# Performance work log

Measured on AMD Instinct MI355X. Metric: run time of the kernel, lower is better.

The kernel has to match this reference:

```python
import jax, jax.numpy as jnp
import numpy as np

N = 50000      # nodes
E = 800000     # edges (avg degree 16)
H = 128        # hidden
ED = 64        # edge_dim
L = 3          # num_layers
LN_EPS = 1e-5


def setup_inputs() -> dict:
    key = jax.random.key(0)
    ks = jax.random.split(key, 12)
    s = jax.random.normal(ks[0], (N, H), dtype=jnp.float32)
    edge_index = jax.random.randint(ks[1], (2, E), 0, N, dtype=jnp.int32)
    edge_attr = jax.random.normal(ks[2], (E, ED), dtype=jnp.float32)
    sc = 0.02
    We = sc * jax.random.normal(ks[3], (L, ED, H), dtype=jnp.float32)
    be = sc * jax.random.normal(ks[4], (L, H), dtype=jnp.float32)
    W1 = sc * jax.random.normal(ks[5], (L, H, H), dtype=jnp.float32)
    b1 = sc * jax.random.normal(ks[6], (L, H), dtype=jnp.float32)
    W2 = sc * jax.random.normal(ks[7], (L, H, H), dtype=jnp.float32)
    b2 = sc * jax.random.normal(ks[8], (L, H), dtype=jnp.float32)
    gamma = jnp.ones((L, H), dtype=jnp.float32)
    beta = jnp.zeros((L, H), dtype=jnp.float32)
    return {"s": s, "edge_index": edge_index, "edge_attr": edge_attr,
            "We": We, "be": be, "W1": W1, "b1": b1, "W2": W2, "b2": b2,
            "gamma": gamma, "beta": beta}


def reference(s, edge_index, edge_attr, We, be, W1, b1, W2, b2, gamma, beta):
    src = edge_index[0]  # j (source of message)
    dst = edge_index[1]  # i (target / aggregation index)
    for l in range(L):
        # GINEConv: message = relu(x_j + Lin(edge_attr)); sum-aggregate; eps=0
        e = edge_attr @ We[l] + be[l]                       # [E, H]
        msg = jax.nn.relu(s[src] + e)                       # [E, H] gather + fuse
        agg = jax.ops.segment_sum(msg, dst, num_segments=N)  # [N, H] scatter-add
        h = s + agg                                         # (1+eps)*x + aggr, eps=0
        h = jax.nn.silu(h @ W1[l] + b1[l]) @ W2[l] + b2[l]   # GINE MLP
        s = s + h                                           # residual
        mu = jnp.mean(s, axis=-1, keepdims=True)
        var = jnp.var(s, axis=-1, keepdims=True)
        s = (s - mu) * jax.lax.rsqrt(var + LN_EPS) * gamma[l] + beta[l]
        s = jax.nn.silu(s)
        # dropout p=0.0 / eval mode -> identity
    return s
```

## Files before the change

### kernel.cpp

```cpp
#include <hip/hip_runtime.h>
#include <hip/hip_bf16.h>

#define HH 128
#define EDD 64
#define NLAYER 3
#define LN_EPS 1e-5f
#define LROW 136

typedef __attribute__((ext_vector_type(8))) __bf16 bf16x8;
typedef __attribute__((ext_vector_type(4))) float f32x4;

static __device__ __forceinline__ float bf2f(unsigned short u) {
    return __uint_as_float(((unsigned)u) << 16);
}
static __device__ __forceinline__ unsigned short f2bf(float f) {
    return __builtin_bit_cast(unsigned short, (__bf16)f);
}
static __device__ __forceinline__ float silu(float x) {
    return x / (1.f + __expf(-x));
}

__global__ __launch_bounds__(256) void hist_kernel(
    const int* __restrict__ dst, int* __restrict__ cnt, int E)
{
    for (int e = blockIdx.x * blockDim.x + threadIdx.x; e < E;
         e += gridDim.x * blockDim.x)
        atomicAdd(&cnt[dst[e]], 1);
}

__global__ __launch_bounds__(1024) void scan_kernel(
    int* __restrict__ cnt_cursor, int* __restrict__ off, int N)
{
    __shared__ int ls[1024];
    const int t = threadIdx.x;
    const int C = (N + 1023) >> 10;
    const int lo = t * C;
    const int hi = min(lo + C, N);
    int sum = 0;
    for (int i = lo; i < hi; ++i) sum += cnt_cursor[i];
    ls[t] = sum;
    __syncthreads();
    for (int d = 1; d < 1024; d <<= 1) {
        int v = (t >= d) ? ls[t - d] : 0;
        __syncthreads();
        ls[t] += v;
        __syncthreads();
    }
    int excl = (t == 0) ? 0 : ls[t - 1];
    for (int i = lo; i < hi; ++i) {
        const int c = cnt_cursor[i];
        off[i] = excl;
        cnt_cursor[i] = excl;
        excl += c;
    }
    if (t == 1023) off[N] = ls[1023];
}

__global__ __launch_bounds__(256) void scatter2_kernel(
    const int* __restrict__ src, const int* __restrict__ dst,
    int* __restrict__ cursor, int* __restrict__ src_s,
    int* __restrict__ eid_s, int E)
{
    if (blockIdx.x == 0 && threadIdx.x < 16) {
        src_s[E + threadIdx.x] = 0;
        eid_s[E + threadIdx.x] = 0;
    }
    for (int e = blockIdx.x * blockDim.x + threadIdx.x; e < E;
         e += gridDim.x * blockDim.x) {
        const int pos = atomicAdd(&cursor[dst[e]], 1);
        src_s[pos] = src[e];
        eid_s[pos] = e;
    }
}

__global__ __launch_bounds__(256) void conv_ea(
    const float* __restrict__ ea, unsigned short* __restrict__ ea_b,
    long long total4)
{
    for (long long i = blockIdx.x * 256LL + threadIdx.x; i < total4;
         i += gridDim.x * 256LL) {
        const float4 v = reinterpret_cast<const float4*>(ea)[i];
        ushort4 o;
        o.x = f2bf(v.x); o.y = f2bf(v.y); o.z = f2bf(v.z); o.w = f2bf(v.w);
        reinterpret_cast<ushort4*>(ea_b)[i] = o;
    }
}

__global__ __launch_bounds__(256) void conv_s(
    const float* __restrict__ s0, unsigned int* __restrict__ sbp,
    long long total4)
{
    for (long long i = blockIdx.x * 256LL + threadIdx.x; i < total4;
         i += gridDim.x * 256LL) {
        const float4 v = reinterpret_cast<const float4*>(s0)[i];
        const unsigned a = (unsigned)f2bf(v.x) | ((unsigned)f2bf(v.y) << 16);
        const unsigned b = (unsigned)f2bf(v.z) | ((unsigned)f2bf(v.w) << 16);
        reinterpret_cast<uint2*>(sbp)[i] = make_uint2(a, b);
    }
}

__global__ void prep_we(const float* __restrict__ We, bf16x8* __restrict__ WeB)
{
    const int t = blockIdx.x * blockDim.x + threadIdx.x;
    if (t >= NLAYER * 16 * 64) return;
    const int lane  = t & 63;
    const int frag  = (t >> 6) & 15;
    const int layer = t >> 10;
    const int kt = frag >> 3, ct = frag & 7;
    const int col = ct * 16 + (lane & 15);
    const int k0  = kt * 32 + (lane >> 4) * 8;
    bf16x8 v;
    #pragma unroll
    for (int j = 0; j < 8; ++j)
        v[j] = (__bf16)We[(long long)layer * EDD * HH + (k0 + j) * HH + col];
    WeB[t] = v;
}

__global__ void prep_w128(const float* __restrict__ W, bf16x8* __restrict__ WB)
{
    const int t = blockIdx.x * blockDim.x + threadIdx.x;
    if (t >= NLAYER * 32 * 64) return;
    const int lane  = t & 63;
    const int frag  = (t >> 6) & 31;
    const int layer = t >> 11;
    const int kt = frag >> 3, ct = frag & 7;
    const int col = ct * 16 + (lane & 15);
    const int k0  = kt * 32 + (lane >> 4) * 8;
    bf16x8 v;
    #pragma unroll
    for (int j = 0; j < 8; ++j)
        v[j] = (__bf16)W[(long long)layer * HH * HH + (k0 + j) * HH + col];
    WB[t] = v;
}

__global__ __launch_bounds__(256, 3) void gine_agg_mfma(
    const float* __restrict__ s,
    const unsigned short* __restrict__ sb,
    const int* __restrict__ src_s,
    const int* __restrict__ eid_s,
    const int* __restrict__ off,
    const unsigned short* __restrict__ ea_b,
    const bf16x8* __restrict__ WeB,
    const float* __restrict__ be,
    unsigned short* __restrict__ hb16,
    int N, int E)
{
    __shared__ unsigned short lsb[2][16 * LROW];

    const int tid  = threadIdx.x;
    const int wave = tid >> 6;
    const int half = wave & 1;
    const int slot = wave >> 1;
    const int lane = tid & 63;
    const int lmod = lane & 15;
    const int ldiv = lane >> 4;

    bf16x8 wb0[4], wb1[4];
    #pragma unroll
    for (int c = 0; c < 4; ++c) {
        wb0[c] = WeB[(0 * 8 + half * 4 + c) * 64 + lane];
        wb1[c] = WeB[(1 * 8 + half * 4 + c) * 64 + lane];
    }
    float bev[4];
    #pragma unroll
    for (int c = 0; c < 4; ++c) bev[c] = be[(half * 4 + c) * 16 + lmod];

    const int st_slot = tid >> 7;
    const int st_row  = (tid >> 3) & 15;
    const int st_su   = (tid & 7) * 16;

    const int stride = gridDim.x * 2;
    int base = blockIdx.x * 2;
    if (base >= N) return;

    int n0 = base;
    int n1 = min(base + 1, N - 1);
    int q0 = off[n0], q0e = off[n0 + 1];
    int q1 = off[n1], q1e = off[n1 + 1];
    int p0  = slot ? q1 : q0;
    int p1  = slot ? q1e : q0e;
    int sp0 = st_slot ? q1 : q0;
    int iters = max(1, max((q0e - q0 + 15) >> 4, (q1e - q1 + 15) >> 4));

    {
        const int snode = src_s[min(sp0 + st_row, E + 15)];
        const unsigned short* srow0 = &sb[(long long)snode * HH + st_su];
        uint4 va = *reinterpret_cast<const uint4*>(srow0);
        uint4 vb = *reinterpret_cast<const uint4*>(srow0 + 8);
        const int rowid = eid_s[min(p0 + lmod, E + 15)];
        const unsigned short* ar = ea_b + (long long)rowid * EDD + ldiv * 8;
        bf16x8 a0 = *reinterpret_cast<const bf16x8*>(ar);
        bf16x8 a1 = *reinterpret_cast<const bf16x8*>(ar + 32);

        while (true) {
            const int nbase = base + stride;
            int nq0 = 0, nq0e = 0, nq1 = 0, nq1e = 0;
            if (nbase < N) {
                const int m0 = nbase, m1 = min(nbase + 1, N - 1);
                nq0 = off[m0]; nq0e = off[m0 + 1];
                nq1 = off[m1]; nq1e = off[m1 + 1];
            }
            const int myn = slot ? n1 : n0;

            float acc[4] = {0.f, 0.f, 0.f, 0.f};

            for (int it = 0; it < iters; ++it) {
                __syncthreads();
                unsigned short* drow = &lsb[st_slot][st_row * LROW + st_su];
                *reinterpret_cast<uint4*>(drow)     = va;
                *reinterpret_cast<uint4*>(drow + 8) = vb;

                uint4 nva = va, nvb = vb;
                bf16x8 na0 = a0, na1 = a1;
                if (it + 1 < iters) {
                    const int ns = src_s[min(sp0 + (it + 1) * 16 + st_row, E + 15)];
                    const unsigned short* nsr = &sb[(long long)ns * HH + st_su];
                    nva = *reinterpret_cast<const uint4*>(nsr);
                    nvb = *reinterpret_cast<const uint4*>(nsr + 8);
                    const int nr = eid_s[min(p0 + (it + 1) * 16 + lmod, E + 15)];
                    const unsigned short* nar = ea_b + (long long)nr * EDD + ldiv * 8;
                    na0 = *reinterpret_cast<const bf16x8*>(nar);
                    na1 = *reinterpret_cast<const bf16x8*>(nar + 32);
                } else if (nbase < N) {
                    const int nsp0 = st_slot ? nq1 : nq0;
                    const int np0  = slot ? nq1 : nq0;
                    const int ns = src_s[min(nsp0 + st_row, E + 15)];
                    const unsigned short* nsr = &sb[(long long)ns * HH + st_su];
                    nva = *reinterpret_cast<const uint4*>(nsr);
                    nvb = *reinterpret_cast<const uint4*>(nsr + 8);
                    const int nr = eid_s[min(np0 + lmod, E + 15)];
                    const unsigned short* nar = ea_b + (long long)nr * EDD + ldiv * 8;
                    na0 = *reinterpret_cast<const bf16x8*>(nar);
                    na1 = *reinterpret_cast<const bf16x8*>(nar + 32);
                }

                f32x4 cf[4];
                #pragma unroll
                for (int c = 0; c < 4; ++c) {
                    f32x4 z = {0.f, 0.f, 0.f, 0.f};
                    z = __builtin_amdgcn_mfma_f32_16x16x32_bf16(a0, wb0[c], z, 0, 0, 0);
                    z = __builtin_amdgcn_mfma_f32_16x16x32_bf16(a1, wb1[c], z, 0, 0, 0);
                    cf[c] = z;
                }

                __syncthreads();

                const int rem = p1 - (p0 + it * 16);
                #pragma unroll
                for (int r = 0; r < 4; ++r) {
                    if (ldiv * 4 + r < rem) {
                        const unsigned short* lr = &lsb[slot][(ldiv * 4 + r) * LROW];
                        #pragma unroll
                        for (int c = 0; c < 4; ++c)
                            acc[c] += fmaxf(
                                bf2f(lr[(half * 4 + c) * 16 + lmod]) + cf[c][r] + bev[c],
                                0.f);
                    }
                }

                va = nva; vb = nvb; a0 = na0; a1 = na1;
            }

            #pragma unroll
            for (int c = 0; c < 4; ++c) {
                acc[c] += __shfl_xor(acc[c], 16, 64);
                acc[c] += __shfl_xor(acc[c], 32, 64);
            }
            const float av = (ldiv == 0) ? acc[0] : (ldiv == 1) ? acc[1]
                           : (ldiv == 2) ? acc[2] : acc[3];
            const int col = (half * 4 + ldiv) * 16 + lmod;
            const long long nb = (long long)myn * HH;
            hb16[nb + col] = f2bf(s[nb + col] + av);

            if (nbase >= N) break;
            base = nbase;
            n0 = base; n1 = min(base + 1, N - 1);
            q0 = nq0; q0e = nq0e; q1 = nq1; q1e = nq1e;
            p0  = slot ? q1 : q0;
            p1  = slot ? q1e : q0e;
            sp0 = st_slot ? q1 : q0;
            iters = max(1, max((q0e - q0 + 15) >> 4, (q1e - q1 + 15) >> 4));
        }
    }
}

__global__ __launch_bounds__(256) void gine_mlp(
    const float* __restrict__ s_in,
    const unsigned short* __restrict__ h16,
    const bf16x8* __restrict__ W1B, const float* __restrict__ b1,
    const bf16x8* __restrict__ W2B, const float* __restrict__ b2,
    const float* __restrict__ gamma, const float* __restrict__ beta,
    float* __restrict__ s_out,
    unsigned short* __restrict__ sb_out,
    int N)
{
    __shared__ unsigned short t1t[16 * LROW];
    __shared__ float2 red[4][16];

    const int wave = threadIdx.x >> 6;
    const int lane = threadIdx.x & 63;
    const int lmod = lane & 15;
    const int ldiv = lane >> 4;

    bf16x8 wf1[4][2], wf2[4][2];
    #pragma unroll
    for (int kt = 0; kt < 4; ++kt) {
        wf1[kt][0] = W1B[(kt * 8 + 2 * wave    ) * 64 + lane];
        wf1[kt][1] = W1B[(kt * 8 + 2 * wave + 1) * 64 + lane];
        wf2[kt][0] = W2B[(kt * 8 + 2 * wave    ) * 64 + lane];
        wf2[kt][1] = W2B[(kt * 8 + 2 * wave + 1) * 64 + lane];
    }
    float4 b1v[2], b2v[2], gv[2], ev[2];
    #pragma unroll
    for (int ctl = 0; ctl < 2; ++ctl) {
        const int oc0 = (2 * wave + ctl) * 16 + ldiv * 4;
        b1v[ctl] = *reinterpret_cast<const float4*>(&b1[oc0]);
        b2v[ctl] = *reinterpret_cast<const float4*>(&b2[oc0]);
        gv[ctl]  = *reinterpret_cast<const float4*>(&gamma[oc0]);
        ev[ctl]  = *reinterpret_cast<const float4*>(&beta[oc0]);
    }

    const int ntiles = (N + 15) >> 4;
    for (int t = blockIdx.x; t < ntiles; t += gridDim.x) {
        const int node = t * 16 + lmod;
        const long long nb = (long long)min(node, N - 1) * HH;

        f32x4 c0 = {0.f, 0.f, 0.f, 0.f};
        f32x4 c1 = {0.f, 0.f, 0.f, 0.f};
        #pragma unroll
        for (int kt = 0; kt < 4; ++kt) {
            const bf16x8 hf = *reinterpret_cast<const bf16x8*>(
                &h16[nb + kt * 32 + ldiv * 8]);
            c0 = __builtin_amdgcn_mfma_f32_16x16x32_bf16(wf1[kt][0], hf, c0, 0, 0, 0);
            c1 = __builtin_amdgcn_mfma_f32_16x16x32_bf16(wf1[kt][1], hf, c1, 0, 0, 0);
        }
        #pragma unroll
        for (int ctl = 0; ctl < 2; ++ctl) {
            const f32x4 cc = ctl ? c1 : c0;
            const float4 bb = ctl ? b1v[1] : b1v[0];
            uint2 pk;
            pk.x = (unsigned)f2bf(silu(cc[0] + bb.x)) |
                   ((unsigned)f2bf(silu(cc[1] + bb.y)) << 16);
            pk.y = (unsigned)f2bf(silu(cc[2] + bb.z)) |
                   ((unsigned)f2bf(silu(cc[3] + bb.w)) << 16);
            const int oc0 = (2 * wave + ctl) * 16 + ldiv * 4;
            *reinterpret_cast<uint2*>(&t1t[lmod * LROW + oc0]) = pk;
        }
        __syncthreads();

        f32x4 d0 = {0.f, 0.f, 0.f, 0.f};
        f32x4 d1 = {0.f, 0.f, 0.f, 0.f};
        #pragma unroll
        for (int kt = 0; kt < 4; ++kt) {
            const bf16x8 tf = *reinterpret_cast<const bf16x8*>(
                &t1t[lmod * LROW + kt * 32 + ldiv * 8]);
            d0 = __builtin_amdgcn_mfma_f32_16x16x32_bf16(wf2[kt][0], tf, d0, 0, 0, 0);
            d1 = __builtin_amdgcn_mfma_f32_16x16x32_bf16(wf2[kt][1], tf, d1, 0, 0, 0);
        }

        float v[2][4];
        float sum = 0.f, ssq = 0.f;
        #pragma unroll
        for (int ctl = 0; ctl < 2; ++ctl) {
            const int oc0 = (2 * wave + ctl) * 16 + ldiv * 4;
            const float4 sv = *reinterpret_cast<const float4*>(&s_in[nb + oc0]);
            const f32x4 dd = ctl ? d1 : d0;
            const float4 bb = ctl ? b2v[1] : b2v[0];
            v[ctl][0] = sv.x + dd[0] + bb.x;
            v[ctl][1] = sv.y + dd[1] + bb.y;
            v[ctl][2] = sv.z + dd[2] + bb.z;
            v[ctl][3] = sv.w + dd[3] + bb.w;
            #pragma unroll
            for (int r = 0; r < 4; ++r) { sum += v[ctl][r]; ssq += v[ctl][r] * v[ctl][r]; }
        }
        sum += __shfl_xor(sum, 16, 64); sum += __shfl_xor(sum, 32, 64);
        ssq += __shfl_xor(ssq, 16, 64); ssq += __shfl_xor(ssq, 32, 64);
        if (ldiv == 0) red[wave][lmod] = make_float2(sum, ssq);
        __syncthreads();
        float ts = 0.f, tq = 0.f;
        #pragma unroll
        for (int w = 0; w < 4; ++w) {
            const float2 rr = red[w][lmod];
            ts += rr.x; tq += rr.y;
        }
        __syncthreads();

        const float mu = ts * (1.0f / HH);
        const float var = tq * (1.0f / HH) - mu * mu;
        const float rs = rsqrtf(var + LN_EPS);

        if (node < N) {
            #pragma unroll
            for (int ctl = 0; ctl < 2; ++ctl) {
                const int oc0 = (2 * wave + ctl) * 16 + ldiv * 4;
                float o[4];
                o[0] = silu((v[ctl][0] - mu) * rs * gv[ctl].x + ev[ctl].x);
                o[1] = silu((v[ctl][1] - mu) * rs * gv[ctl].y + ev[ctl].y);
                o[2] = silu((v[ctl][2] - mu) * rs * gv[ctl].z + ev[ctl].z);
                o[3] = silu((v[ctl][3] - mu) * rs * gv[ctl].w + ev[ctl].w);
                *reinterpret_cast<float4*>(&s_out[nb + oc0]) =
                    make_float4(o[0], o[1], o[2], o[3]);
                uint2 pk;
                pk.x = (unsigned)f2bf(o[0]) | ((unsigned)f2bf(o[1]) << 16);
                pk.y = (unsigned)f2bf(o[2]) | ((unsigned)f2bf(o[3]) << 16);
                *reinterpret_cast<uint2*>(&sb_out[nb + oc0]) = pk;
            }
        }
    }
}

extern "C" void kernel_launch(void* const* d_in, const int* in_sizes, int n_in,
                              void* d_out, int out_size, void* d_ws, size_t ws_size,
                              hipStream_t stream) {
    const float* s0  = (const float*)d_in[0];
    const int*   ei  = (const int*)  d_in[1];
    const float* ea  = (const float*)d_in[2];
    const float* We  = (const float*)d_in[3];
    const float* be  = (const float*)d_in[4];
    const float* W1  = (const float*)d_in[5];
    const float* b1  = (const float*)d_in[6];
    const float* W2  = (const float*)d_in[7];
    const float* b2  = (const float*)d_in[8];
    const float* gm  = (const float*)d_in[9];
    const float* bt  = (const float*)d_in[10];

    const int NH = in_sizes[0];
    const int N  = NH / HH;
    const int E  = in_sizes[1] / 2;
    const int* src = ei;
    const int* dst = ei + E;

    float*          sbuf  = (float*)d_ws;
    unsigned short* sb    = (unsigned short*)(sbuf + NH);
    unsigned short* hb16  = sb + NH;
    unsigned short* ea_b  = hb16 + NH;
    bf16x8*         WeB   = (bf16x8*)(ea_b + (size_t)E * EDD);
    bf16x8*         W1B   = WeB + NLAYER * 16 * 64;
    bf16x8*         W2B   = W1B + NLAYER * 32 * 64;
    int*            src_s = (int*)(W2B + NLAYER * 32 * 64);
    int*            eid_s = src_s + (E + 16);
    int*            off   = eid_s + (E + 16);
    int*            cursor= off + (N + 1);

    hipMemsetAsync(cursor, 0, sizeof(int) * N, stream);
    hist_kernel<<<1024, 256, 0, stream>>>(dst, cursor, E);
    scan_kernel<<<1, 1024, 0, stream>>>(cursor, off, N);
    scatter2_kernel<<<1024, 256, 0, stream>>>(src, dst, cursor, src_s, eid_s, E);
    conv_ea<<<2048, 256, 0, stream>>>(ea, ea_b, (long long)E * EDD / 4);
    conv_s<<<1024, 256, 0, stream>>>(s0, (unsigned int*)sb, (long long)NH / 4);
    prep_we<<<12, 256, 0, stream>>>(We, WeB);
    prep_w128<<<24, 256, 0, stream>>>(W1, W1B);
    prep_w128<<<24, 256, 0, stream>>>(W2, W2B);

    for (int l = 0; l < NLAYER; ++l) {
        const float* scur = (l == 0) ? s0 : sbuf;
        gine_agg_mfma<<<4096, 256, 0, stream>>>(scur, sb, src_s, eid_s, off, ea_b,
                                                WeB + (size_t)l * 16 * 64,
                                                be + l * HH, hb16, N, E);
        float* sout = (l == NLAYER - 1) ? (float*)d_out : sbuf;
        gine_mlp<<<2048, 256, 0, stream>>>(scur, hb16,
                                           W1B + (size_t)l * 32 * 64, b1 + l * HH,
                                           W2B + (size_t)l * 32 * 64, b2 + l * HH,
                                           gm + l * HH, bt + l * HH,
                                           sout, sb, N);
    }
}
```

Baseline: 615.5 us.

## Store bf16 edge attributes in destination-sorted order, drop edge-id indirection

The edge-attribute conversion now writes each bf16 row to its CSR (dst-sorted) position, using a per-edge position array recorded during the scatter pass. The aggregation kernel then reads edge attributes contiguously by sorted position instead of gathering through an edge-id array. This removes one indirect index load and turns random 128-byte row gathers into sequential reads in each of the three layers. The cost is a scattered write in the one-time conversion kernel, and 16 padding rows that must be zeroed with an extra memset.

```diff
diff --git a/kernel.cpp b/kernel.cpp
--- a/kernel.cpp
+++ b/kernel.cpp
@@ -56,33 +56,31 @@
     if (t == 1023) off[N] = ls[1023];
 }
 
-__global__ __launch_bounds__(256) void scatter2_kernel(
+__global__ __launch_bounds__(256) void scatter3_kernel(
     const int* __restrict__ src, const int* __restrict__ dst,
     int* __restrict__ cursor, int* __restrict__ src_s,
-    int* __restrict__ eid_s, int E)
-{
-    if (blockIdx.x == 0 && threadIdx.x < 16) {
+    int* __restrict__ pos_e, int E)
+{
+    if (blockIdx.x == 0 && threadIdx.x < 16)
         src_s[E + threadIdx.x] = 0;
-        eid_s[E + threadIdx.x] = 0;
-    }
     for (int e = blockIdx.x * blockDim.x + threadIdx.x; e < E;
          e += gridDim.x * blockDim.x) {
         const int pos = atomicAdd(&cursor[dst[e]], 1);
         src_s[pos] = src[e];
-        eid_s[pos] = e;
-    }
-}
-
-__global__ __launch_bounds__(256) void conv_ea(
-    const float* __restrict__ ea, unsigned short* __restrict__ ea_b,
-    long long total4)
-{
-    for (long long i = blockIdx.x * 256LL + threadIdx.x; i < total4;
-         i += gridDim.x * 256LL) {
-        const float4 v = reinterpret_cast<const float4*>(ea)[i];
-        ushort4 o;
-        o.x = f2bf(v.x); o.y = f2bf(v.y); o.z = f2bf(v.z); o.w = f2bf(v.w);
-        reinterpret_cast<ushort4*>(ea_b)[i] = o;
+        pos_e[e] = pos;
+    }
+}
+
+__global__ __launch_bounds__(256) void conv_ea_sorted(
+    const float* __restrict__ ea, const int* __restrict__ pos_e,
+    unsigned short* __restrict__ ea_s, int E)
+{
+    const int wave = threadIdx.x >> 6;
+    const int lane = threadIdx.x & 63;
+    for (int e = blockIdx.x * 4 + wave; e < E; e += gridDim.x * 4) {
+        const float v = ea[(long long)e * EDD + lane];
+        const int pos = pos_e[e];
+        ea_s[(long long)pos * EDD + lane] = f2bf(v);
     }
 }
 
@@ -137,9 +135,8 @@
     const float* __restrict__ s,
     const unsigned short* __restrict__ sb,
     const int* __restrict__ src_s,
-    const int* __restrict__ eid_s,
     const int* __restrict__ off,
-    const unsigned short* __restrict__ ea_b,
+    const unsigned short* __restrict__ ea_s,
     const bf16x8* __restrict__ WeB,
     const float* __restrict__ be,
     unsigned short* __restrict__ hb16,
@@ -187,8 +184,8 @@
         const unsigned short* srow0 = &sb[(long long)snode * HH + st_su];
         uint4 va = *reinterpret_cast<const uint4*>(srow0);
         uint4 vb = *reinterpret_cast<const uint4*>(srow0 + 8);
-        const int rowid = eid_s[min(p0 + lmod, E + 15)];
-        const unsigned short* ar = ea_b + (long long)rowid * EDD + ldiv * 8;
+        const unsigned short* ar =
+            ea_s + (long long)min(p0 + lmod, E + 15) * EDD + ldiv * 8;
         bf16x8 a0 = *reinterpret_cast<const bf16x8*>(ar);
         bf16x8 a1 = *reinterpret_cast<const bf16x8*>(ar + 32);
 
@@ -217,8 +214,9 @@
                     const unsigned short* nsr = &sb[(long long)ns * HH + st_su];
                     nva = *reinterpret_cast<const uint4*>(nsr);
                     nvb = *reinterpret_cast<const uint4*>(nsr + 8);
-                    const int nr = eid_s[min(p0 + (it + 1) * 16 + lmod, E + 15)];
-                    const unsigned short* nar = ea_b + (long long)nr * EDD + ldiv * 8;
+                    const unsigned short* nar =
+                        ea_s + (long long)min(p0 + (it + 1) * 16 + lmod, E + 15) * EDD
+                        + ldiv * 8;
                     na0 = *reinterpret_cast<const bf16x8*>(nar);
                     na1 = *reinterpret_cast<const bf16x8*>(nar + 32);
                 } else if (nbase < N) {
@@ -228,8 +226,8 @@
                     const unsigned short* nsr = &sb[(long long)ns * HH + st_su];
                     nva = *reinterpret_cast<const uint4*>(nsr);
                     nvb = *reinterpret_cast<const uint4*>(nsr + 8);
-                    const int nr = eid_s[min(np0 + lmod, E + 15)];
-                    const unsigned short* nar = ea_b + (long long)nr * EDD + ldiv * 8;
+                    const unsigned short* nar =
+                        ea_s + (long long)min(np0 + lmod, E + 15) * EDD + ldiv * 8;
                     na0 = *reinterpret_cast<const bf16x8*>(nar);
                     na1 = *reinterpret_cast<const bf16x8*>(nar + 32);
                 }
@@ -433,20 +431,21 @@
     float*          sbuf  = (float*)d_ws;
     unsigned short* sb    = (unsigned short*)(sbuf + NH);
     unsigned short* hb16  = sb + NH;
-    unsigned short* ea_b  = hb16 + NH;
-    bf16x8*         WeB   = (bf16x8*)(ea_b + (size_t)E * EDD);
+    unsigned short* ea_s  = hb16 + NH;
+    bf16x8*         WeB   = (bf16x8*)(ea_s + (size_t)(E + 16) * EDD);
     bf16x8*         W1B   = WeB + NLAYER * 16 * 64;
     bf16x8*         W2B   = W1B + NLAYER * 32 * 64;
     int*            src_s = (int*)(W2B + NLAYER * 32 * 64);
-    int*            eid_s = src_s + (E + 16);
-    int*            off   = eid_s + (E + 16);
+    int*            pos_e = src_s + (E + 16);
+    int*            off   = pos_e + E;
     int*            cursor= off + (N + 1);
 
     hipMemsetAsync(cursor, 0, sizeof(int) * N, stream);
+    hipMemsetAsync(ea_s + (size_t)E * EDD, 0, 16 * EDD * sizeof(unsigned short), stream);
     hist_kernel<<<1024, 256, 0, stream>>>(dst, cursor, E);
     scan_kernel<<<1, 1024, 0, stream>>>(cursor, off, N);
-    scatter2_kernel<<<1024, 256, 0, stream>>>(src, dst, cursor, src_s, eid_s, E);
-    conv_ea<<<2048, 256, 0, stream>>>(ea, ea_b, (long long)E * EDD / 4);
+    scatter3_kernel<<<1024, 256, 0, stream>>>(src, dst, cursor, src_s, pos_e, E);
+    conv_ea_sorted<<<2048, 256, 0, stream>>>(ea, pos_e, ea_s, E);
     conv_s<<<1024, 256, 0, stream>>>(s0, (unsigned int*)sb, (long long)NH / 4);
     prep_we<<<12, 256, 0, stream>>>(We, WeB);
     prep_w128<<<24, 256, 0, stream>>>(W1, W1B);
@@ -454,7 +453,7 @@
 
     for (int l = 0; l < NLAYER; ++l) {
         const float* scur = (l == 0) ? s0 : sbuf;
-        gine_agg_mfma<<<4096, 256, 0, stream>>>(scur, sb, src_s, eid_s, off, ea_b,
+        gine_agg_mfma<<<4096, 256, 0, stream>>>(scur, sb, src_s, off, ea_s,
                                                 WeB + (size_t)l * 16 * 64,
                                                 be + l * HH, hb16, N, E);
         float* sout = (l == NLAYER - 1) ? (float*)d_out : sbuf;
```

Result: slower. 635.1 us (+3.2%).
